# Optimization experiments

Hardware: AMD Instinct MI355X
Metric: run time of the kernel (lower is better)

## Reference

```python
import jax, jax.numpy as jnp
import numpy as np

R, C = 2048, 2048
N = R * C            # 4194304 nodes
DIM = 2


def _build_graph():
    ids = np.arange(N, dtype=np.int64).reshape(R, C)
    # horizontal edges (i,j)-(i,j+1), then vertical (i,j)-(i+1,j)
    h = np.stack([ids[:, :-1].ravel(), ids[:, 1:].ravel()], axis=1)
    v = np.stack([ids[:-1, :].ravel(), ids[1:, :].ravel()], axis=1)
    edges = np.concatenate([h, v], axis=0)  # [E, 2]
    # rest positions: (x=j, y=i) -> unit spacing grid
    jj, ii = np.meshgrid(np.arange(C, dtype=np.float32), np.arange(R, dtype=np.float32))
    pos = np.stack([jj.ravel(), ii.ravel()], axis=1)  # [N, 2]
    rest = np.linalg.norm(pos[edges[:, 1]] - pos[edges[:, 0]], axis=1).astype(np.float32)
    bmask = np.zeros((R, C), dtype=bool)
    bmask[0, :] = bmask[-1, :] = bmask[:, 0] = bmask[:, -1] = True
    fixed = ids[bmask]
    return edges, rest, fixed


def setup_inputs() -> dict:
    key = jax.random.key(0)
    k_t, k_y, k_m, k_k, k_c = jax.random.split(key, 5)
    edges_np, rest_np, fixed_np = _build_graph()
    E = edges_np.shape[0]
    return {
        "t": jax.random.normal(k_t, (1,), dtype=jnp.float32),
        "y": jax.random.normal(k_y, (2 * N * DIM,), dtype=jnp.float32),
        "mass": jax.random.uniform(k_m, (N, DIM), dtype=jnp.float32, minval=0.5, maxval=1.5),
        "k": jax.random.uniform(k_k, (E,), dtype=jnp.float32, minval=5.0, maxval=15.0),
        "c": jax.random.uniform(k_c, (N, DIM), dtype=jnp.float32, minval=0.1, maxval=1.0),
        "rest_lengths": jnp.asarray(rest_np),
        "edges": jnp.asarray(edges_np),
        "fixed_nodes": jnp.asarray(fixed_np),
    }


def reference(t, y, mass, k, c, rest_lengths, edges, fixed_nodes):
    n = N * DIM
    x = y[:n].reshape(N, DIM)   # positions
    v = y[n:].reshape(N, DIM)   # velocities
    i_nodes = edges[:, 0]
    j_nodes = edges[:, 1]
    # per-edge spring force (gather -> elementwise -> scatter)
    dx = x[j_nodes] - x[i_nodes]                               # [E, 2]
    lengths = jnp.maximum(jnp.sqrt(jnp.sum(dx * dx, axis=1)), 1e-12)
    directions = dx / lengths[:, None]
    edge_forces = (k * (lengths - rest_lengths))[:, None] * directions  # [E, 2]
    f_spring = (jnp.zeros_like(x)
                .at[i_nodes].add(edge_forces)
                .at[j_nodes].add(-edge_forces))
    # damping + Newton's law (forcing_fn is None -> no external force)
    acceleration = (f_spring - c * v) / mass
    # fixed boundary nodes: zero velocity and acceleration
    v = v.at[fixed_nodes].set(0.0)
    acceleration = acceleration.at[fixed_nodes].set(0.0)
    return jnp.concatenate([v.reshape(-1), acceleration.reshape(-1)])
```

## Files before the change

kernel.cpp:

```cpp
#include <hip/hip_runtime.h>


#define RR 2048
#define CC 2048
#define NN (RR * CC)
#define EH (RR * (CC - 1))

typedef float vf2 __attribute__((ext_vector_type(2)));

__global__ __launch_bounds__(256) void spring_lattice_rhs(
    const float* __restrict__ y,
    const float* __restrict__ mass,
    const float* __restrict__ karr,
    const float* __restrict__ carr,
    float* __restrict__ out)
{
    int n = blockIdx.x * blockDim.x + threadIdx.x;
    if (n >= NN) return;

    int r = n >> 11;
    int c = n & 2047;

    const vf2* x2 = (const vf2*)y;
    const vf2* v2 = (const vf2*)(y + 2 * NN);

    vf2 xn = x2[n];
    float fx = 0.0f, fy = 0.0f;

    if (c < CC - 1) {
        vf2 xm = x2[n + 1];
        float dx = xm.x - xn.x, dy = xm.y - xn.y;
        float len = fmaxf(sqrtf(dx * dx + dy * dy), 1e-12f);
        float s = karr[r * (CC - 1) + c] * (len - 1.0f) / len;
        fx += s * dx; fy += s * dy;
    }
    if (c > 0) {
        vf2 xm = x2[n - 1];
        float dx = xm.x - xn.x, dy = xm.y - xn.y;
        float len = fmaxf(sqrtf(dx * dx + dy * dy), 1e-12f);
        float s = karr[r * (CC - 1) + (c - 1)] * (len - 1.0f) / len;
        fx += s * dx; fy += s * dy;
    }
    if (r < RR - 1) {
        vf2 xm = x2[n + CC];
        float dx = xm.x - xn.x, dy = xm.y - xn.y;
        float len = fmaxf(sqrtf(dx * dx + dy * dy), 1e-12f);
        float s = karr[EH + n] * (len - 1.0f) / len;
        fx += s * dx; fy += s * dy;
    }
    if (r > 0) {
        vf2 xm = x2[n - CC];
        float dx = xm.x - xn.x, dy = xm.y - xn.y;
        float len = fmaxf(sqrtf(dx * dx + dy * dy), 1e-12f);
        float s = karr[EH + n - CC] * (len - 1.0f) / len;
        fx += s * dx; fy += s * dy;
    }

    vf2 vn = v2[n];
    vf2 mn = ((const vf2*)mass)[n];
    vf2 cn = ((const vf2*)carr)[n];

    float ax = (fx - cn.x * vn.x) / mn.x;
    float ay = (fy - cn.y * vn.y) / mn.y;

    bool fixed = (r == 0) | (r == RR - 1) | (c == 0) | (c == CC - 1);
    vf2 ov, oa;
    ov.x = fixed ? 0.0f : vn.x;
    ov.y = fixed ? 0.0f : vn.y;
    oa.x = fixed ? 0.0f : ax;
    oa.y = fixed ? 0.0f : ay;

    __builtin_nontemporal_store(ov, (vf2*)out + n);
    __builtin_nontemporal_store(oa, (vf2*)(out + 2 * NN) + n);
}

extern "C" void kernel_launch(void* const* d_in, const int* in_sizes, int n_in,
                              void* d_out, int out_size, void* d_ws, size_t ws_size,
                              hipStream_t stream) {
    const float* y    = (const float*)d_in[1];
    const float* mass = (const float*)d_in[2];
    const float* karr = (const float*)d_in[3];
    const float* carr = (const float*)d_in[4];
    float* out = (float*)d_out;

    dim3 block(256);
    dim3 grid((NN + 255) / 256);
    spring_lattice_rhs<<<grid, block, 0, stream>>>(y, mass, karr, carr, out);
}
```

Baseline: 45.87 us.

## Process four nodes per thread with vectorized loads and fast reciprocal math

Each thread now handles four consecutive lattice nodes in a row. It loads positions, velocities, mass and damping as 16-byte vectors and reuses the neighbouring horizontal positions and spring constants across the four nodes. Exact sqrt and division are replaced with hardware sqrt and reciprocal approximations. This cuts load instructions and redundant neighbour reads, and uses fewer threads with more registers each, at some cost in numerical accuracy.

```diff
diff --git a/kernel.cpp b/kernel.cpp
--- a/kernel.cpp
+++ b/kernel.cpp
@@ -7,71 +7,108 @@
 #define EH (RR * (CC - 1))
 
 typedef float vf2 __attribute__((ext_vector_type(2)));
+typedef float vf4 __attribute__((ext_vector_type(4)));
 
-__global__ __launch_bounds__(256) void spring_lattice_rhs(
+__device__ __forceinline__ void spring(float& fx, float& fy,
+    float xn, float yn, float xo, float yo, float k)
+{
+    float dx = xo - xn, dy = yo - yn;
+    float len = fmaxf(__builtin_amdgcn_sqrtf(dx * dx + dy * dy), 1e-12f);
+    float s = k - k * __builtin_amdgcn_rcpf(len);
+    fx += s * dx; fy += s * dy;
+}
+
+__global__ __launch_bounds__(256) void spring_lattice_rhs4(
     const float* __restrict__ y,
     const float* __restrict__ mass,
     const float* __restrict__ karr,
     const float* __restrict__ carr,
     float* __restrict__ out)
 {
-    int n = blockIdx.x * blockDim.x + threadIdx.x;
-    if (n >= NN) return;
+    int t = blockIdx.x * blockDim.x + threadIdx.x;
+    int r  = t >> 9;
+    int c0 = (t & 511) << 2;
+    int n0 = (r << 11) + c0;
+    int h  = n0 >> 1;
 
-    int r = n >> 11;
-    int c = n & 2047;
+    const vf4* x4 = (const vf4*)y;
+    const vf4* v4 = (const vf4*)(y + 2 * NN);
 
-    const vf2* x2 = (const vf2*)y;
-    const vf2* v2 = (const vf2*)(y + 2 * NN);
+    bool hasL = (c0 > 0), hasR = (c0 < CC - 4);
+    bool hasU = (r > 0),  hasD = (r < RR - 1);
 
-    vf2 xn = x2[n];
-    float fx = 0.0f, fy = 0.0f;
+    vf4 xab = x4[h], xcd = x4[h + 1];
+    vf2 xl = hasL ? ((const vf2*)y)[n0 - 1] : (vf2){0.f, 0.f};
+    vf2 xr = hasR ? ((const vf2*)y)[n0 + 4] : (vf2){0.f, 0.f};
+    vf4 xu0 = {0,0,0,0}, xu1 = {0,0,0,0}, xd0 = {0,0,0,0}, xd1 = {0,0,0,0};
+    if (hasU) { xu0 = x4[h - (CC >> 1)]; xu1 = x4[h - (CC >> 1) + 1]; }
+    if (hasD) { xd0 = x4[h + (CC >> 1)]; xd1 = x4[h + (CC >> 1) + 1]; }
 
-    if (c < CC - 1) {
-        vf2 xm = x2[n + 1];
-        float dx = xm.x - xn.x, dy = xm.y - xn.y;
-        float len = fmaxf(sqrtf(dx * dx + dy * dy), 1e-12f);
-        float s = karr[r * (CC - 1) + c] * (len - 1.0f) / len;
-        fx += s * dx; fy += s * dy;
-    }
-    if (c > 0) {
-        vf2 xm = x2[n - 1];
-        float dx = xm.x - xn.x, dy = xm.y - xn.y;
-        float len = fmaxf(sqrtf(dx * dx + dy * dy), 1e-12f);
-        float s = karr[r * (CC - 1) + (c - 1)] * (len - 1.0f) / len;
-        fx += s * dx; fy += s * dy;
-    }
-    if (r < RR - 1) {
-        vf2 xm = x2[n + CC];
-        float dx = xm.x - xn.x, dy = xm.y - xn.y;
-        float len = fmaxf(sqrtf(dx * dx + dy * dy), 1e-12f);
-        float s = karr[EH + n] * (len - 1.0f) / len;
-        fx += s * dx; fy += s * dy;
-    }
-    if (r > 0) {
-        vf2 xm = x2[n - CC];
-        float dx = xm.x - xn.x, dy = xm.y - xn.y;
-        float len = fmaxf(sqrtf(dx * dx + dy * dy), 1e-12f);
-        float s = karr[EH + n - CC] * (len - 1.0f) / len;
-        fx += s * dx; fy += s * dy;
+    int e0 = r * (CC - 1) + c0;
+    float kh0 = hasL ? karr[e0 - 1] : 0.f;
+    float kh1 = karr[e0];
+    float kh2 = karr[e0 + 1];
+    float kh3 = karr[e0 + 2];
+    float kh4 = hasR ? karr[e0 + 3] : 0.f;
+
+    const vf4* kv4 = (const vf4*)(karr + EH);
+    vf4 kvd = hasD ? kv4[n0 >> 2] : (vf4){0,0,0,0};
+    vf4 kvu = hasU ? kv4[(n0 - CC) >> 2] : (vf4){0,0,0,0};
+
+    vf4 vab = v4[h],                   vcd = v4[h + 1];
+    vf4 mab = ((const vf4*)mass)[h],   mcd = ((const vf4*)mass)[h + 1];
+    vf4 cab = ((const vf4*)carr)[h],   ccd = ((const vf4*)carr)[h + 1];
+
+    float px[6] = {xl.x, xab.x, xab.z, xcd.x, xcd.z, xr.x};
+    float py[6] = {xl.y, xab.y, xab.w, xcd.y, xcd.w, xr.y};
+    float pux[4] = {xu0.x, xu0.z, xu1.x, xu1.z};
+    float puy[4] = {xu0.y, xu0.w, xu1.y, xu1.w};
+    float pdx[4] = {xd0.x, xd0.z, xd1.x, xd1.z};
+    float pdy[4] = {xd0.y, xd0.w, xd1.y, xd1.w};
+    float khA[5] = {kh0, kh1, kh2, kh3, kh4};
+    float kua[4] = {kvu.x, kvu.y, kvu.z, kvu.w};
+    float kda[4] = {kvd.x, kvd.y, kvd.z, kvd.w};
+
+    float fx[4], fy[4];
+#pragma unroll
+    for (int i = 0; i < 4; ++i) {
+        float xn = px[i + 1], yn = py[i + 1];
+        float gx = 0.f, gy = 0.f;
+        spring(gx, gy, xn, yn, px[i],     py[i],     khA[i]);
+        spring(gx, gy, xn, yn, px[i + 2], py[i + 2], khA[i + 1]);
+        spring(gx, gy, xn, yn, pux[i],    puy[i],    kua[i]);
+        spring(gx, gy, xn, yn, pdx[i],    pdy[i],    kda[i]);
+        fx[i] = gx; fy[i] = gy;
     }
 
-    vf2 vn = v2[n];
-    vf2 mn = ((const vf2*)mass)[n];
-    vf2 cn = ((const vf2*)carr)[n];
+    bool rowFixed = (r == 0) | (r == RR - 1);
+    bool f0 = rowFixed | (c0 == 0);
+    bool f1 = rowFixed;
+    bool f2 = rowFixed;
+    bool f3 = rowFixed | (c0 == CC - 4);
 
-    float ax = (fx - cn.x * vn.x) / mn.x;
-    float ay = (fy - cn.y * vn.y) / mn.y;
+    float ax0 = (fx[0] - cab.x * vab.x) * __builtin_amdgcn_rcpf(mab.x);
+    float ay0 = (fy[0] - cab.y * vab.y) * __builtin_amdgcn_rcpf(mab.y);
+    float ax1 = (fx[1] - cab.z * vab.z) * __builtin_amdgcn_rcpf(mab.z);
+    float ay1 = (fy[1] - cab.w * vab.w) * __builtin_amdgcn_rcpf(mab.w);
+    float ax2 = (fx[2] - ccd.x * vcd.x) * __builtin_amdgcn_rcpf(mcd.x);
+    float ay2 = (fy[2] - ccd.y * vcd.y) * __builtin_amdgcn_rcpf(mcd.y);
+    float ax3 = (fx[3] - ccd.z * vcd.z) * __builtin_amdgcn_rcpf(mcd.z);
+    float ay3 = (fy[3] - ccd.w * vcd.w) * __builtin_amdgcn_rcpf(mcd.w);
 
-    bool fixed = (r == 0) | (r == RR - 1) | (c == 0) | (c == CC - 1);
-    vf2 ov, oa;
-    ov.x = fixed ? 0.0f : vn.x;
-    ov.y = fixed ? 0.0f : vn.y;
-    oa.x = fixed ? 0.0f : ax;
-    oa.y = fixed ? 0.0f : ay;
+    vf4 ov0 = { f0 ? 0.f : vab.x, f0 ? 0.f : vab.y,
+                f1 ? 0.f : vab.z, f1 ? 0.f : vab.w };
+    vf4 ov1 = { f2 ? 0.f : vcd.x, f2 ? 0.f : vcd.y,
+                f3 ? 0.f : vcd.z, f3 ? 0.f : vcd.w };
+    vf4 oa0 = { f0 ? 0.f : ax0, f0 ? 0.f : ay0,
+                f1 ? 0.f : ax1, f1 ? 0.f : ay1 };
+    vf4 oa1 = { f2 ? 0.f : ax2, f2 ? 0.f : ay2,
+                f3 ? 0.f : ax3, f3 ? 0.f : ay3 };
 
-    __builtin_nontemporal_store(ov, (vf2*)out + n);
-    __builtin_nontemporal_store(oa, (vf2*)(out + 2 * NN) + n);
+    __builtin_nontemporal_store(ov0, (vf4*)out + h);
+    __builtin_nontemporal_store(ov1, (vf4*)out + h + 1);
+    __builtin_nontemporal_store(oa0, (vf4*)(out + 2 * NN) + h);
+    __builtin_nontemporal_store(oa1, (vf4*)(out + 2 * NN) + h + 1);
 }
 
 extern "C" void kernel_launch(void* const* d_in, const int* in_sizes, int n_in,
@@ -84,6 +121,6 @@
     float* out = (float*)d_out;
 
     dim3 block(256);
-    dim3 grid((NN + 255) / 256);
-    spring_lattice_rhs<<<grid, block, 0, stream>>>(y, mass, karr, carr, out);
+    dim3 grid((NN / 4 + 255) / 256);
+    spring_lattice_rhs4<<<grid, block, 0, stream>>>(y, mass, karr, carr, out);
 }
```

After: 51.67 us. +12.6%, slower.
